# Performance work log

Measured on AMD Instinct MI355X. Metric: run time of the kernel, lower is better.

## Reference

```python
import jax, jax.numpy as jnp
import numpy as np

N = 50000      # cells (nodes)
E = 1600000    # directed edges (kNN connectivity graph)
F_IN = 2000    # highly-variable genes
HID = 16
H = 4          # GAT heads
C = 16         # GAT out channels per head
NUM_CLASSES = 3


def setup_inputs() -> dict:
    key = jax.random.key(0)
    ks = jax.random.split(key, 10)
    x = jax.random.normal(ks[0], (N, F_IN), dtype=jnp.float32)
    edge_index = jax.random.randint(ks[1], (2, E), 0, N, dtype=jnp.int64)
    s = 0.05
    W1 = jax.random.normal(ks[2], (F_IN, HID), dtype=jnp.float32) * s
    b1 = jnp.zeros((HID,), jnp.float32)
    Wg = jax.random.normal(ks[3], (HID, H * C), dtype=jnp.float32) * s
    att_src = jax.random.normal(ks[4], (H, C), dtype=jnp.float32) * s
    att_dst = jax.random.normal(ks[5], (H, C), dtype=jnp.float32) * s
    bg = jnp.zeros((H * C,), jnp.float32)
    Wo = jax.random.normal(ks[6], (H * C, NUM_CLASSES), dtype=jnp.float32) * s
    bo = jnp.zeros((NUM_CLASSES,), jnp.float32)
    return {"x": x, "edge_index": edge_index, "W1": W1, "b1": b1, "Wg": Wg,
            "att_src": att_src, "att_dst": att_dst, "bg": bg, "Wo": Wo, "bo": bo}


def reference(x, edge_index, W1, b1, Wg, att_src, att_dst, bg, Wo, bo):
    n = x.shape[0]
    loops = jnp.arange(n, dtype=edge_index.dtype)
    src = jnp.concatenate([edge_index[0], loops])  # [E+N]
    dst = jnp.concatenate([edge_index[1], loops])

    # ---- GCNConv(F_IN -> 16): project, symmetric-normalize, scatter-add ----
    h = x @ W1                                                   # [N, 16]
    deg = jax.ops.segment_sum(jnp.ones(src.shape, h.dtype), dst, num_segments=n)
    dinv = jnp.where(deg > 0, jax.lax.rsqrt(deg), 0.0)
    norm = dinv[src] * dinv[dst]                                 # [E+N]
    h = jax.ops.segment_sum(h[src] * norm[:, None], dst, num_segments=n) + b1
    h = jax.nn.relu(h)                                           # dropout is identity in eval

    # ---- GATConv(16 -> 16, heads=4, concat) ----
    g = (h @ Wg).reshape(n, H, C)                                # [N, H, C]
    a_s = jnp.einsum('nhc,hc->nh', g, att_src)                   # [N, H]
    a_d = jnp.einsum('nhc,hc->nh', g, att_dst)
    e = jax.nn.leaky_relu(a_s[src] + a_d[dst], 0.2)              # [E+N, H]
    m = jax.ops.segment_max(e, dst, num_segments=n)              # segment softmax (stable)
    ex = jnp.exp(e - m[dst])
    denom = jax.ops.segment_sum(ex, dst, num_segments=n)
    alpha = ex / (denom[dst] + 1e-16)                            # [E+N, H]
    out = jax.ops.segment_sum(g[src] * alpha[:, :, None], dst, num_segments=n)
    out = out.reshape(n, H * C) + bg                             # [N, 64]

    # ---- classifier head ----
    logits = out @ Wo + bo                                       # [N, 3]
    return jax.nn.log_softmax(logits, axis=1)
```

## Files before the change

### kernel.cpp

```cpp
#include <hip/hip_runtime.h>
#include <hip/hip_bf16.h>
#include <math.h>

#define F_IN   2000
#define HID    16
#define HEADS  4
#define CPH    16
#define HC     64
#define NCLS   3

__device__ __forceinline__ float lrelu(float x){ return x > 0.f ? x : 0.2f*x; }

__device__ __forceinline__ float comp4(const float4& v, int k){
  return k==0 ? v.x : k==1 ? v.y : k==2 ? v.z : v.w;
}

__device__ __forceinline__ float bf2f(unsigned short u){
  return __uint_as_float(((unsigned)u) << 16);
}

__global__ void k_zero(int* __restrict__ deg, int n) {
  int i = blockIdx.x * 256 + threadIdx.x;
  if (i < n) deg[i] = 0;
}

__global__ __launch_bounds__(256) void k_gemm1(const float* __restrict__ x,
                                               const float* __restrict__ W1,
                                               __hip_bfloat16* __restrict__ h0b,
                                               int n) {
  const int t    = threadIdx.x;
  const int lane = t & 63;
  const int wid  = t >> 6;
  const int rowbase = blockIdx.x * 16 + wid * 4;
  const float4* __restrict__ w1f4 = reinterpret_cast<const float4*>(W1);

  float acc[64];
  #pragma unroll
  for (int v = 0; v < 64; ++v) acc[v] = 0.f;

  float4 xc[4], xn[4];

  auto loadx = [&](float4* xv, int ci) {
    const int f4l = ci * 64 + lane;
    const bool kv = (f4l < 500);
    #pragma unroll
    for (int r = 0; r < 4; ++r) {
      int row = rowbase + r;
      xv[r] = (kv && row < n)
          ? *reinterpret_cast<const float4*>(x + (size_t)row * F_IN + f4l * 4)
          : make_float4(0.f, 0.f, 0.f, 0.f);
    }
  };

  loadx(xc, 0);

  for (int ci = 0; ci < 8; ++ci) {
    if (ci < 7) loadx(xn, ci + 1);
    const int f4l = ci * 64 + lane;
    const int kc = (f4l < 500) ? f4l : 0;
    #pragma unroll
    for (int kk = 0; kk < 4; ++kk) {
      const int k = 4 * kc + kk;
      float4 w0 = w1f4[k * 4 + 0];
      float4 w1v = w1f4[k * 4 + 1];
      float4 w2 = w1f4[k * 4 + 2];
      float4 w3 = w1f4[k * 4 + 3];
      #pragma unroll
      for (int r = 0; r < 4; ++r) {
        float xk = comp4(xc[r], kk);
        acc[r*16+ 0] += xk * w0.x;  acc[r*16+ 1] += xk * w0.y;
        acc[r*16+ 2] += xk * w0.z;  acc[r*16+ 3] += xk * w0.w;
        acc[r*16+ 4] += xk * w1v.x; acc[r*16+ 5] += xk * w1v.y;
        acc[r*16+ 6] += xk * w1v.z; acc[r*16+ 7] += xk * w1v.w;
        acc[r*16+ 8] += xk * w2.x;  acc[r*16+ 9] += xk * w2.y;
        acc[r*16+10] += xk * w2.z;  acc[r*16+11] += xk * w2.w;
        acc[r*16+12] += xk * w3.x;  acc[r*16+13] += xk * w3.y;
        acc[r*16+14] += xk * w3.z;  acc[r*16+15] += xk * w3.w;
      }
    }
    if (ci < 7) {
      #pragma unroll
      for (int r = 0; r < 4; ++r) xc[r] = xn[r];
    }
  }

  #pragma unroll
  for (int b = 32; b >= 1; b >>= 1) {
    bool hi = (lane & b) != 0;
    #pragma unroll
    for (int j = 0; j < b; ++j) {
      float send = hi ? acc[j] : acc[b + j];
      float recv = __shfl_xor(send, b);
      acc[j] = (hi ? acc[b + j] : acc[j]) + recv;
    }
  }
  int r = lane >> 4, c = lane & 15;
  int row = rowbase + r;
  if (row < n) h0b[(size_t)row * 16 + c] = __float2bfloat16(acc[0]);
}

__global__ void k_deg(const int* __restrict__ edst, int* __restrict__ deg, int e) {
  int i = blockIdx.x * 256 + threadIdx.x;
  if (i < e) atomicAdd(&deg[edst[i]], 1);
}

__global__ void k_scan_a(const int* __restrict__ deg, int* __restrict__ bsum, int n) {
  __shared__ int s[256];
  int i = blockIdx.x * 256 + threadIdx.x;
  s[threadIdx.x] = (i < n) ? deg[i] : 0;
  __syncthreads();
  for (int off = 128; off > 0; off >>= 1) {
    if (threadIdx.x < off) s[threadIdx.x] += s[threadIdx.x + off];
    __syncthreads();
  }
  if (threadIdx.x == 0) bsum[blockIdx.x] = s[0];
}

__global__ void k_scan_b(int* __restrict__ bsum, int nb) {
  int lane = threadIdx.x;
  int carry = 0;
  for (int base = 0; base < nb; base += 64) {
    int idx = base + lane;
    int orig = (idx < nb) ? bsum[idx] : 0;
    int v = orig;
    #pragma unroll
    for (int off = 1; off < 64; off <<= 1) {
      int tv = __shfl_up(v, off);
      if (lane >= off) v += tv;
    }
    if (idx < nb) bsum[idx] = carry + v - orig;
    carry += __shfl(v, 63);
  }
}

__global__ void k_scan_c(const int* __restrict__ deg, const int* __restrict__ bsum,
                         int* __restrict__ rowptr, int* __restrict__ cursor,
                         float* __restrict__ dinv, int n) {
  __shared__ int s[256];
  int i = blockIdx.x * 256 + threadIdx.x;
  int v = (i < n) ? deg[i] : 0;
  s[threadIdx.x] = v;
  __syncthreads();
  for (int off = 1; off < 256; off <<= 1) {
    int tv = (threadIdx.x >= off) ? s[threadIdx.x - off] : 0;
    __syncthreads();
    s[threadIdx.x] += tv;
    __syncthreads();
  }
  int excl = s[threadIdx.x] - v + bsum[blockIdx.x];
  if (i < n) {
    rowptr[i] = excl;
    cursor[i] = excl;
    dinv[i] = rsqrtf((float)(v + 1));
    if (i == n - 1) rowptr[n] = excl + v;
  }
}

__global__ void k_scatter(const int* __restrict__ esrc, const int* __restrict__ edst,
                          int* __restrict__ cursor, int* __restrict__ csr, int e) {
  int i = blockIdx.x * 256 + threadIdx.x;
  if (i < e) {
    int d = edst[i];
    int pos = atomicAdd(&cursor[d], 1);
    csr[pos] = esrc[i];
  }
}

__global__ __launch_bounds__(256) void k_gcn(
    const unsigned short* __restrict__ h0b, const int* __restrict__ rowptr,
    const int* __restrict__ csr, const float* __restrict__ dinv,
    const float* __restrict__ b1, const float* __restrict__ Wg,
    const float* __restrict__ atts, const float* __restrict__ attd,
    __hip_bfloat16* __restrict__ gb, float* __restrict__ a_s,
    float* __restrict__ a_d, int n) {
  __shared__ float wgs[HID * HC];
  __shared__ float ats[HC], atd[HC];
  int t = threadIdx.x;
  for (int i = t; i < HID * HC; i += 256) wgs[i] = Wg[i];
  if (t < HC) { ats[t] = atts[t]; atd[t] = attd[t]; }
  __syncthreads();

  int lane = t & 63, w = t >> 6;
  int dst = blockIdx.x * 4 + w;
  if (dst >= n) return;
  int j = lane >> 4, c = lane & 15;
  int start = rowptr[dst], end = rowptr[dst + 1];
  float dd = dinv[dst];

  float acc = 0.f;
  for (int idx = start + j; idx < end; idx += 4) {
    int src = csr[idx];
    acc += bf2f(h0b[(size_t)src * 16 + c]) * dinv[src];
  }
  acc += __shfl_xor(acc, 16);
  acc += __shfl_xor(acc, 32);
  acc = acc * dd + bf2f(h0b[(size_t)dst * 16 + c]) * dd * dd;
  float hv = fmaxf(acc + b1[c], 0.f);

  float go = 0.f;
  #pragma unroll
  for (int k = 0; k < 16; ++k) {
    float hk = __shfl(hv, k);
    go += hk * wgs[k * HC + lane];
  }
  gb[(size_t)dst * HC + lane] = __float2bfloat16(go);

  float asv = go * ats[lane], adv = go * atd[lane];
  #pragma unroll
  for (int m = 1; m < 16; m <<= 1) {
    asv += __shfl_xor(asv, m);
    adv += __shfl_xor(adv, m);
  }
  if (c == 0) {
    a_s[(size_t)dst * 4 + j] = asv;
    a_d[(size_t)dst * 4 + j] = adv;
  }
}

__global__ __launch_bounds__(256) void k_gat(
    const unsigned short* __restrict__ gb, const int* __restrict__ rowptr,
    const int* __restrict__ csr, const float* __restrict__ a_s,
    const float* __restrict__ a_d, const float* __restrict__ bg,
    const float* __restrict__ Wo, const float* __restrict__ bo,
    float* __restrict__ out, int n) {
  __shared__ float wos[HC * NCLS];
  __shared__ float bgs[HC];
  __shared__ float bos[NCLS];
  int t = threadIdx.x;
  if (t < HC * NCLS) wos[t] = Wo[t];
  if (t < HC) bgs[t] = bg[t];
  if (t < NCLS) bos[t] = bo[t];
  __syncthreads();

  int lane = t & 63, w = t >> 6;
  int dst = blockIdx.x * 4 + w;
  if (dst >= n) return;
  int start = rowptr[dst], end = rowptr[dst + 1];
  int j = lane >> 4, c = lane & 15, h = c >> 2;

  float adh = a_d[(size_t)dst * 4 + h];
  float ash = a_s[(size_t)dst * 4 + h];

  float m = -1e30f, den = 0.f;
  float a0 = 0.f, a1 = 0.f, a2 = 0.f, a3 = 0.f;

  for (int idx = start + j; idx < end; idx += 4) {
    int src = csr[idx];
    float e = lrelu(a_s[(size_t)src * 4 + h] + adh);
    float mn = fmaxf(m, e);
    float corr = __expf(m - mn);
    float p = __expf(e - mn);
    ushort4 u4 = *reinterpret_cast<const ushort4*>(gb + (size_t)src * HC + c * 4);
    den = den * corr + p;
    a0 = a0 * corr + p * bf2f(u4.x);
    a1 = a1 * corr + p * bf2f(u4.y);
    a2 = a2 * corr + p * bf2f(u4.z);
    a3 = a3 * corr + p * bf2f(u4.w);
    m = mn;
  }
  if (j == 0) {
    float e = lrelu(ash + adh);
    float mn = fmaxf(m, e);
    float corr = __expf(m - mn);
    float p = __expf(e - mn);
    ushort4 u4 = *reinterpret_cast<const ushort4*>(gb + (size_t)dst * HC + c * 4);
    den = den * corr + p;
    a0 = a0 * corr + p * bf2f(u4.x);
    a1 = a1 * corr + p * bf2f(u4.y);
    a2 = a2 * corr + p * bf2f(u4.z);
    a3 = a3 * corr + p * bf2f(u4.w);
    m = mn;
  }

  #pragma unroll
  for (int msk = 16; msk <= 32; msk <<= 1) {
    float m2 = __shfl_xor(m, msk);
    float d2 = __shfl_xor(den, msk);
    float b0 = __shfl_xor(a0, msk);
    float b1v = __shfl_xor(a1, msk);
    float b2 = __shfl_xor(a2, msk);
    float b3 = __shfl_xor(a3, msk);
    float M = fmaxf(m, m2);
    float c1 = __expf(m - M), c2 = __expf(m2 - M);
    den = den * c1 + d2 * c2;
    a0 = a0 * c1 + b0 * c2;
    a1 = a1 * c1 + b1v * c2;
    a2 = a2 * c1 + b2 * c2;
    a3 = a3 * c1 + b3 * c2;
    m = M;
  }
  den += 1e-16f;

  float o0 = a0 / den + bgs[c * 4 + 0];
  float o1 = a1 / den + bgs[c * 4 + 1];
  float o2 = a2 / den + bgs[c * 4 + 2];
  float o3 = a3 / den + bgs[c * 4 + 3];

  float p0 = 0.f, p1 = 0.f, p2 = 0.f;
  {
    int ch = c * 4;
    p0 += o0 * wos[(ch+0)*NCLS+0] + o1 * wos[(ch+1)*NCLS+0] + o2 * wos[(ch+2)*NCLS+0] + o3 * wos[(ch+3)*NCLS+0];
    p1 += o0 * wos[(ch+0)*NCLS+1] + o1 * wos[(ch+1)*NCLS+1] + o2 * wos[(ch+2)*NCLS+1] + o3 * wos[(ch+3)*NCLS+1];
    p2 += o0 * wos[(ch+0)*NCLS+2] + o1 * wos[(ch+1)*NCLS+2] + o2 * wos[(ch+2)*NCLS+2] + o3 * wos[(ch+3)*NCLS+2];
  }
  #pragma unroll
  for (int msk = 1; msk < 16; msk <<= 1) {
    p0 += __shfl_xor(p0, msk);
    p1 += __shfl_xor(p1, msk);
    p2 += __shfl_xor(p2, msk);
  }
  p0 += bos[0]; p1 += bos[1]; p2 += bos[2];
  float mx = fmaxf(p0, fmaxf(p1, p2));
  float ls = mx + logf(__expf(p0 - mx) + __expf(p1 - mx) + __expf(p2 - mx));
  if (lane == 0) {
    out[(size_t)dst * 3 + 0] = p0 - ls;
    out[(size_t)dst * 3 + 1] = p1 - ls;
    out[(size_t)dst * 3 + 2] = p2 - ls;
  }
}

extern "C" void kernel_launch(void* const* d_in, const int* in_sizes, int n_in,
                              void* d_out, int out_size, void* d_ws, size_t ws_size,
                              hipStream_t stream) {
  const float* x    = (const float*)d_in[0];
  const int*   ei   = (const int*)  d_in[1];
  const float* W1   = (const float*)d_in[2];
  const float* b1   = (const float*)d_in[3];
  const float* Wg   = (const float*)d_in[4];
  const float* atts = (const float*)d_in[5];
  const float* attd = (const float*)d_in[6];
  const float* bg   = (const float*)d_in[7];
  const float* Wo   = (const float*)d_in[8];
  const float* bo   = (const float*)d_in[9];
  float* out = (float*)d_out;

  const int n = in_sizes[0] / F_IN;
  const int e = in_sizes[1] / 2;
  const int* esrc = ei;
  const int* edst = ei + e;

  char* p = (char*)d_ws;
  auto alloc = [&](size_t bytes) { char* r = p; p += (bytes + 255) & ~(size_t)255; return r; };
  __hip_bfloat16* h0b = (__hip_bfloat16*)alloc((size_t)n * 16 * 2);
  int*   deg    = (int*)  alloc((size_t)n * 4);
  int*   cursor = (int*)  alloc((size_t)n * 4);
  float* dinv   = (float*)alloc((size_t)n * 4);
  int*   rowptr = (int*)  alloc((size_t)(n + 1) * 4);
  int*   bsum   = (int*)  alloc(4096);
  int*   csr    = (int*)  alloc((size_t)e * 4);
  __hip_bfloat16* gbuf = (__hip_bfloat16*)alloc((size_t)n * HC * 2);
  float* as_    = (float*)alloc((size_t)n * 4 * 4);
  float* ad_    = (float*)alloc((size_t)n * 4 * 4);

  int nzb = (n + 255) / 256;
  k_zero<<<nzb, 256, 0, stream>>>(deg, n);

  k_gemm1<<<(n + 15) / 16, 256, 0, stream>>>(x, W1, h0b, n);

  k_deg<<<(e + 255) / 256, 256, 0, stream>>>(edst, deg, e);

  int nb = (n + 255) / 256;
  k_scan_a<<<nb, 256, 0, stream>>>(deg, bsum, n);
  k_scan_b<<<1, 64, 0, stream>>>(bsum, nb);
  k_scan_c<<<nb, 256, 0, stream>>>(deg, bsum, rowptr, cursor, dinv, n);

  k_scatter<<<(e + 255) / 256, 256, 0, stream>>>(esrc, edst, cursor, csr, e);

  k_gcn<<<(n + 3) / 4, 256, 0, stream>>>((const unsigned short*)h0b, rowptr, csr,
                                         dinv, b1, Wg, atts, attd,
                                         gbuf, as_, ad_, n);

  k_gat<<<(n + 3) / 4, 256, 0, stream>>>((const unsigned short*)gbuf, rowptr, csr,
                                         as_, ad_, bg, Wo, bo, out, n);
}
```

Measured before the change: 542.2 us.

## Stage W1 chunks in swizzled shared memory and triple-buffer x loads in GEMM1

The first projection GEMM now copies W1 into LDS in four 500-row chunks with a bank-rotating swizzle. The loads for the next chunk are staged through registers, and block barriers guard the write. Rows of x are prefetched two chunk-steps ahead with a three-deep register buffer instead of one. The aim is to stop every lane streaming distinct W1 rows through the vector cache and to hide more of the x stream's latency. In exchange it adds LDS use, extra barriers and register pressure, and it drops the row<n bounds guard.

```diff
diff --git a/kernel.cpp b/kernel.cpp
--- a/kernel.cpp
+++ b/kernel.cpp
@@ -28,59 +28,87 @@
                                                const float* __restrict__ W1,
                                                __hip_bfloat16* __restrict__ h0b,
                                                int n) {
+  __shared__ float w1s[8192];
   const int t    = threadIdx.x;
   const int lane = t & 63;
   const int wid  = t >> 6;
   const int rowbase = blockIdx.x * 16 + wid * 4;
-  const float4* __restrict__ w1f4 = reinterpret_cast<const float4*>(W1);
 
   float acc[64];
   #pragma unroll
   for (int v = 0; v < 64; ++v) acc[v] = 0.f;
 
-  float4 xc[4], xn[4];
-
-  auto loadx = [&](float4* xv, int ci) {
-    const int f4l = ci * 64 + lane;
-    const bool kv = (f4l < 500);
+  float4 sreg[8];
+  float4 xs[3][4];
+
+  auto stage_load = [&](int p) {
+    const size_t kbase = (size_t)p * 500 * 16;
+    #pragma unroll
+    for (int b = 0; b < 8; ++b) {
+      int f = t + 256 * b;
+      int fc = (f < 2000) ? f : 1999;
+      sreg[b] = *reinterpret_cast<const float4*>(W1 + kbase + (size_t)fc * 4);
+    }
+  };
+  auto stage_write = [&]() {
+    #pragma unroll
+    for (int b = 0; b < 8; ++b) {
+      int f = t + 256 * b;
+      int k = f >> 2, q = f & 3;
+      int qs = (q + (k >> 2)) & 3;
+      float4 v = (f < 2000) ? sreg[b] : make_float4(0.f, 0.f, 0.f, 0.f);
+      *reinterpret_cast<float4*>(w1s + k * 16 + qs * 4) = v;
+    }
+  };
+  auto loadxs = [&](float4* xv, int ci) {
+    const int f4l = (ci & 1) * 64 + lane;
+    const bool kv = (f4l < 125);
+    const int base = (ci >> 1) * 500 + f4l * 4;
     #pragma unroll
     for (int r = 0; r < 4; ++r) {
-      int row = rowbase + r;
-      xv[r] = (kv && row < n)
-          ? *reinterpret_cast<const float4*>(x + (size_t)row * F_IN + f4l * 4)
-          : make_float4(0.f, 0.f, 0.f, 0.f);
+      xv[r] = kv ? *reinterpret_cast<const float4*>(x + (size_t)(rowbase + r) * F_IN + base)
+                 : make_float4(0.f, 0.f, 0.f, 0.f);
     }
   };
-
-  loadx(xc, 0);
-
+  auto compute = [&](const float4* xv, int ci) {
+    const int f4l = (ci & 1) * 64 + lane;
+    #pragma unroll
+    for (int kk = 0; kk < 4; ++kk) {
+      const int rs = 4 * f4l + kk;
+      const float* rowp = w1s + rs * 16;
+      float xk0 = comp4(xv[0], kk), xk1 = comp4(xv[1], kk);
+      float xk2 = comp4(xv[2], kk), xk3 = comp4(xv[3], kk);
+      #pragma unroll
+      for (int q = 0; q < 4; ++q) {
+        const int qs = (q + f4l) & 3;
+        float4 w4 = *reinterpret_cast<const float4*>(rowp + (qs << 2));
+        acc[0*16+4*q+0] += xk0 * w4.x; acc[0*16+4*q+1] += xk0 * w4.y;
+        acc[0*16+4*q+2] += xk0 * w4.z; acc[0*16+4*q+3] += xk0 * w4.w;
+        acc[1*16+4*q+0] += xk1 * w4.x; acc[1*16+4*q+1] += xk1 * w4.y;
+        acc[1*16+4*q+2] += xk1 * w4.z; acc[1*16+4*q+3] += xk1 * w4.w;
+        acc[2*16+4*q+0] += xk2 * w4.x; acc[2*16+4*q+1] += xk2 * w4.y;
+        acc[2*16+4*q+2] += xk2 * w4.z; acc[2*16+4*q+3] += xk2 * w4.w;
+        acc[3*16+4*q+0] += xk3 * w4.x; acc[3*16+4*q+1] += xk3 * w4.y;
+        acc[3*16+4*q+2] += xk3 * w4.z; acc[3*16+4*q+3] += xk3 * w4.w;
+      }
+    }
+  };
+
+  stage_load(0);
+  loadxs(xs[0], 0);
+  loadxs(xs[1], 1);
+  stage_write();
+  __syncthreads();
+
+  #pragma unroll
   for (int ci = 0; ci < 8; ++ci) {
-    if (ci < 7) loadx(xn, ci + 1);
-    const int f4l = ci * 64 + lane;
-    const int kc = (f4l < 500) ? f4l : 0;
-    #pragma unroll
-    for (int kk = 0; kk < 4; ++kk) {
-      const int k = 4 * kc + kk;
-      float4 w0 = w1f4[k * 4 + 0];
-      float4 w1v = w1f4[k * 4 + 1];
-      float4 w2 = w1f4[k * 4 + 2];
-      float4 w3 = w1f4[k * 4 + 3];
-      #pragma unroll
-      for (int r = 0; r < 4; ++r) {
-        float xk = comp4(xc[r], kk);
-        acc[r*16+ 0] += xk * w0.x;  acc[r*16+ 1] += xk * w0.y;
-        acc[r*16+ 2] += xk * w0.z;  acc[r*16+ 3] += xk * w0.w;
-        acc[r*16+ 4] += xk * w1v.x; acc[r*16+ 5] += xk * w1v.y;
-        acc[r*16+ 6] += xk * w1v.z; acc[r*16+ 7] += xk * w1v.w;
-        acc[r*16+ 8] += xk * w2.x;  acc[r*16+ 9] += xk * w2.y;
-        acc[r*16+10] += xk * w2.z;  acc[r*16+11] += xk * w2.w;
-        acc[r*16+12] += xk * w3.x;  acc[r*16+13] += xk * w3.y;
-        acc[r*16+14] += xk * w3.z;  acc[r*16+15] += xk * w3.w;
-      }
-    }
-    if (ci < 7) {
-      #pragma unroll
-      for (int r = 0; r < 4; ++r) xc[r] = xn[r];
+    if ((ci & 1) == 0 && ci < 6) stage_load((ci >> 1) + 1);
+    if (ci < 6) loadxs(xs[(ci + 2) % 3], ci + 2);
+    compute(xs[ci % 3], ci);
+    if ((ci & 1) == 1 && ci < 7) {
+      __syncthreads();
+      stage_write();
+      __syncthreads();
     }
   }
 
```

Result: faster. 490.5 us (-9.5%).
